# Performance work log

Hardware: AMD Instinct MI355X
Metric: run time of the kernel (lower is better)

The kernel has to match this reference:

```python
import jax, jax.numpy as jnp
import numpy as np

NEG = jnp.float32(-9e15)
SLOPE = 0.2  # LeakyReLU negative slope used in LocalAggregator


def setup_inputs() -> dict:
    key = jax.random.key(0)
    k1, k2, k3, k4, k5, k6, k7 = jax.random.split(key, 7)
    B, N, D, V = 32, 200, 100, 50000
    stdv = 1.0 / np.sqrt(D)
    inputs = jax.random.randint(k1, (B, N), 0, V)
    adj = jax.random.randint(k2, (B, N, N), 0, 5).astype(jnp.int32)
    mask_item = jnp.ones((B, N), dtype=jnp.int32)
    emb = jax.random.uniform(k3, (V, D), jnp.float32, -stdv, stdv)
    a0 = jax.random.uniform(k4, (D, 1), jnp.float32, -stdv, stdv)
    a1 = jax.random.uniform(k5, (D, 1), jnp.float32, -stdv, stdv)
    a2 = jax.random.uniform(k6, (D, 1), jnp.float32, -stdv, stdv)
    a3 = jax.random.uniform(k7, (D, 1), jnp.float32, -stdv, stdv)
    return {"inputs": inputs, "adj": adj, "mask_item": mask_item,
            "emb": emb, "a0": a0, "a1": a1, "a2": a2, "a3": a3}


def reference(inputs, adj, mask_item, emb, a0, a1, a2, a3):
    # h: [B, N, D] session item embeddings
    h = emb[inputs]
    # e_k[b,i,j] = leaky_relu(sum_d h[b,i,d]*h[b,j,d]*a_k[d])
    # (equivalent to the original (h_i * h_j) @ a_k without the BxNxNxD blowup)
    def edge_score(a):
        s = jnp.einsum('bid,bjd->bij', h * a[:, 0][None, None, :], h)
        return jax.nn.leaky_relu(s, SLOPE)
    e0, e1, e2, e3 = edge_score(a0), edge_score(a1), edge_score(a2), edge_score(a3)
    alpha = jnp.where(adj == 1, e0, NEG)
    alpha = jnp.where(adj == 2, e1, alpha)
    alpha = jnp.where(adj == 3, e2, alpha)
    alpha = jnp.where(adj == 4, e3, alpha)
    alpha = jax.nn.softmax(alpha, axis=-1)  # [B, N, N]
    # weighted aggregation over neighbors; dropout_local is inactive in eval
    return jnp.einsum('bij,bjd->bid', alpha, h)
```

## Files before the change

### kernel.cpp

```cpp
#include <hip/hip_runtime.h>
#include <math.h>

#define NEGV (-9e15f)
#define SLOPE 0.2f

__global__ __launch_bounds__(256, 1) void gat_tile_kernel(
    const int*   __restrict__ inputs,
    const int*   __restrict__ adj,
    const float* __restrict__ emb,
    const float* __restrict__ a0, const float* __restrict__ a1,
    const float* __restrict__ a2, const float* __restrict__ a3,
    float*       __restrict__ out)
{
    const int b   = blockIdx.x >> 3;
    const int i0  = (blockIdx.x & 7) * 25;
    const int tid = threadIdx.x;

    __shared__ int   sidx[200];
    __shared__ float G[25][4][100];
    __shared__ float ST[200][28];

    if (tid < 200) sidx[tid] = inputs[b * 200 + tid];
    __syncthreads();

    const float4* embv = (const float4*)emb;

    for (int t = tid; t < 25 * 25; t += 256) {
        const int i = t / 25, dc = t % 25;
        const float4 hv = embv[(size_t)sidx[i0 + i] * 25 + dc];
        const float4 av0 = ((const float4*)a0)[dc];
        const float4 av1 = ((const float4*)a1)[dc];
        const float4 av2 = ((const float4*)a2)[dc];
        const float4 av3 = ((const float4*)a3)[dc];
        float4 g;
        g.x=hv.x*av0.x; g.y=hv.y*av0.y; g.z=hv.z*av0.z; g.w=hv.w*av0.w;
        ((float4*)&G[i][0][0])[dc] = g;
        g.x=hv.x*av1.x; g.y=hv.y*av1.y; g.z=hv.z*av1.z; g.w=hv.w*av1.w;
        ((float4*)&G[i][1][0])[dc] = g;
        g.x=hv.x*av2.x; g.y=hv.y*av2.y; g.z=hv.z*av2.z; g.w=hv.w*av2.w;
        ((float4*)&G[i][2][0])[dc] = g;
        g.x=hv.x*av3.x; g.y=hv.y*av3.y; g.z=hv.z*av3.z; g.w=hv.w*av3.w;
        ((float4*)&G[i][3][0])[dc] = g;
    }

    float4 h[25];
    int    kv[25];
    if (tid < 200) {
        const size_t hb = (size_t)sidx[tid] * 25;
        #pragma unroll
        for (int c = 0; c < 25; ++c) h[c] = embv[hb + c];
        const int arow = (b * 200 + i0) * 200 + tid;
        #pragma unroll
        for (int i = 0; i < 25; ++i) kv[i] = adj[arow + i * 200];
    }
    __syncthreads();

    if (tid < 200) {
        for (int i = 0; i < 25; ++i) {
            const int k  = kv[i];
            const int kk = (k - 1) & 3;
            const float4* Gv = (const float4*)&G[i][kk][0];
            float ax = 0.f, ay = 0.f, az = 0.f, aw = 0.f;
            #pragma unroll
            for (int c = 0; c < 25; ++c) {
                const float4 gv = Gv[c];
                ax += gv.x * h[c].x; ay += gv.y * h[c].y;
                az += gv.z * h[c].z; aw += gv.w * h[c].w;
            }
            float s = (ax + ay) + (az + aw);
            s = (s >= 0.f) ? s : SLOPE * s;
            ST[tid][i] = (k >= 1 && k <= 4) ? s : NEGV;
        }
    }
    __syncthreads();

    {
        const int r = tid >> 3, l = tid & 7;
        if (r < 25) {
            float m = -INFINITY;
            #pragma unroll
            for (int t = 0; t < 25; ++t) m = fmaxf(m, ST[l + 8 * t][r]);
            #pragma unroll
            for (int off = 4; off >= 1; off >>= 1) m = fmaxf(m, __shfl_xor(m, off, 8));
            float e[25];
            float sum = 0.f;
            #pragma unroll
            for (int t = 0; t < 25; ++t) {
                e[t] = __expf(ST[l + 8 * t][r] - m);
                sum += e[t];
            }
            #pragma unroll
            for (int off = 4; off >= 1; off >>= 1) sum += __shfl_xor(sum, off, 8);
            const float inv = 1.0f / sum;
            #pragma unroll
            for (int t = 0; t < 25; ++t) ST[l + 8 * t][r] = e[t] * inv;
        }
    }
    __syncthreads();

    {
        const int ig = tid & 7;
        const int dc = tid >> 3;
        float4 acc[25];
        #pragma unroll
        for (int i = 0; i < 25; ++i) { acc[i].x = 0.f; acc[i].y = 0.f; acc[i].z = 0.f; acc[i].w = 0.f; }
        if (dc < 25) {
            for (int jj = 0; jj < 25; ++jj) {
                const int j = ig * 25 + jj;
                float4 w4[7];
                #pragma unroll
                for (int c = 0; c < 7; ++c) w4[c] = ((const float4*)&ST[j][0])[c];
                const float* w = (const float*)w4;
                const float4 hv = embv[(size_t)sidx[j] * 25 + dc];
                #pragma unroll
                for (int i = 0; i < 25; ++i) {
                    acc[i].x += w[i] * hv.x; acc[i].y += w[i] * hv.y;
                    acc[i].z += w[i] * hv.z; acc[i].w += w[i] * hv.w;
                }
            }
        }
        #pragma unroll
        for (int i = 0; i < 25; ++i) {
            #pragma unroll
            for (int off = 1; off <= 4; off <<= 1) {
                acc[i].x += __shfl_xor(acc[i].x, off, 64);
                acc[i].y += __shfl_xor(acc[i].y, off, 64);
                acc[i].z += __shfl_xor(acc[i].z, off, 64);
                acc[i].w += __shfl_xor(acc[i].w, off, 64);
            }
        }
        if (ig == 0 && dc < 25) {
            #pragma unroll
            for (int i = 0; i < 25; ++i)
                ((float4*)out)[(size_t)(b * 200 + i0 + i) * 25 + dc] = acc[i];
        }
    }
}

extern "C" void kernel_launch(void* const* d_in, const int* in_sizes, int n_in,
                              void* d_out, int out_size, void* d_ws, size_t ws_size,
                              hipStream_t stream) {
    const int*   inputs = (const int*)  d_in[0];
    const int*   adj    = (const int*)  d_in[1];
    const float* emb    = (const float*)d_in[3];
    const float* a0     = (const float*)d_in[4];
    const float* a1     = (const float*)d_in[5];
    const float* a2     = (const float*)d_in[6];
    const float* a3     = (const float*)d_in[7];
    float*       out    = (float*)d_out;

    gat_tile_kernel<<<dim3(256), dim3(256), 0, stream>>>(inputs, adj, emb, a0, a1, a2, a3, out);
}
```

Measured before the change: 111.3 us.

## Rewrite GAT kernel with fp16 MFMA scores and 16-row tiles

Replaces the scalar fp32 score computation with fp16 MFMA 16x16x32 matrix instructions over all four attention vectors, retiles to 16 query rows per block (416 blocks), caches the gathered embeddings as fp16 in shared memory, and stores softmax weights in fp16 for the aggregation step. The aim is to cut ALU time in the dot-product phase and raise grid occupancy. In exchange it computes four score matrices instead of selecting one per edge, and it loses precision in the scores, weights and embeddings.

Result: faster. 106.1 us (-4.7%).

```diff
diff --git a/kernel.cpp b/kernel.cpp
--- a/kernel.cpp
+++ b/kernel.cpp
@@ -1,10 +1,15 @@
 #include <hip/hip_runtime.h>
 #include <math.h>
 
-#define NEGV (-9e15f)
+#define NEGV  (-9e15f)
 #define SLOPE 0.2f
 
-__global__ __launch_bounds__(256, 1) void gat_tile_kernel(
+typedef __fp16 f16;
+typedef __fp16 f16x4 __attribute__((ext_vector_type(4)));
+typedef __fp16 f16x8 __attribute__((ext_vector_type(8)));
+typedef float  f32x4 __attribute__((ext_vector_type(4)));
+
+__global__ __launch_bounds__(256) void gat_mfma_kernel(
     const int*   __restrict__ inputs,
     const int*   __restrict__ adj,
     const float* __restrict__ emb,
@@ -12,127 +17,212 @@
     const float* __restrict__ a2, const float* __restrict__ a3,
     float*       __restrict__ out)
 {
-    const int b   = blockIdx.x >> 3;
-    const int i0  = (blockIdx.x & 7) * 25;
+    const int b   = blockIdx.x / 13;
+    const int i0  = (blockIdx.x % 13) * 16;
     const int tid = threadIdx.x;
 
+    __shared__ f16 HF[200][112];
+    __shared__ __align__(16) unsigned char ubuf[4 * 16 * 96 * 2];
+    __shared__ f16 GT[4][16][32];
     __shared__ int   sidx[200];
-    __shared__ float G[25][4][100];
-    __shared__ float ST[200][28];
-
-    if (tid < 200) sidx[tid] = inputs[b * 200 + tid];
-    __syncthreads();
-
-    const float4* embv = (const float4*)emb;
-
-    for (int t = tid; t < 25 * 25; t += 256) {
-        const int i = t / 25, dc = t % 25;
-        const float4 hv = embv[(size_t)sidx[i0 + i] * 25 + dc];
-        const float4 av0 = ((const float4*)a0)[dc];
-        const float4 av1 = ((const float4*)a1)[dc];
-        const float4 av2 = ((const float4*)a2)[dc];
-        const float4 av3 = ((const float4*)a3)[dc];
-        float4 g;
-        g.x=hv.x*av0.x; g.y=hv.y*av0.y; g.z=hv.z*av0.z; g.w=hv.w*av0.w;
-        ((float4*)&G[i][0][0])[dc] = g;
-        g.x=hv.x*av1.x; g.y=hv.y*av1.y; g.z=hv.z*av1.z; g.w=hv.w*av1.w;
-        ((float4*)&G[i][1][0])[dc] = g;
-        g.x=hv.x*av2.x; g.y=hv.y*av2.y; g.z=hv.z*av2.z; g.w=hv.w*av2.w;
-        ((float4*)&G[i][2][0])[dc] = g;
-        g.x=hv.x*av3.x; g.y=hv.y*av3.y; g.z=hv.z*av3.z; g.w=hv.w*av3.w;
-        ((float4*)&G[i][3][0])[dc] = g;
-    }
-
-    float4 h[25];
-    int    kv[25];
+    __shared__ float redmax[16][4];
+    __shared__ float redsum[16][4];
+
+    f16 (*GF)[16][96] = (f16(*)[16][96])ubuf;
+    f16 (*ST)[24]     = (f16(*)[24])ubuf;
+
+    for (int t = tid; t < 200; t += 256) sidx[t] = inputs[b * 200 + t];
+    __syncthreads();
+
     if (tid < 200) {
-        const size_t hb = (size_t)sidx[tid] * 25;
-        #pragma unroll
-        for (int c = 0; c < 25; ++c) h[c] = embv[hb + c];
-        const int arow = (b * 200 + i0) * 200 + tid;
-        #pragma unroll
-        for (int i = 0; i < 25; ++i) kv[i] = adj[arow + i * 200];
-    }
-    __syncthreads();
-
-    if (tid < 200) {
-        for (int i = 0; i < 25; ++i) {
-            const int k  = kv[i];
-            const int kk = (k - 1) & 3;
-            const float4* Gv = (const float4*)&G[i][kk][0];
-            float ax = 0.f, ay = 0.f, az = 0.f, aw = 0.f;
-            #pragma unroll
-            for (int c = 0; c < 25; ++c) {
-                const float4 gv = Gv[c];
-                ax += gv.x * h[c].x; ay += gv.y * h[c].y;
-                az += gv.z * h[c].z; aw += gv.w * h[c].w;
-            }
-            float s = (ax + ay) + (az + aw);
-            s = (s >= 0.f) ? s : SLOPE * s;
-            ST[tid][i] = (k >= 1 && k <= 4) ? s : NEGV;
-        }
-    }
-    __syncthreads();
-
-    {
-        const int r = tid >> 3, l = tid & 7;
-        if (r < 25) {
-            float m = -INFINITY;
-            #pragma unroll
-            for (int t = 0; t < 25; ++t) m = fmaxf(m, ST[l + 8 * t][r]);
-            #pragma unroll
-            for (int off = 4; off >= 1; off >>= 1) m = fmaxf(m, __shfl_xor(m, off, 8));
-            float e[25];
-            float sum = 0.f;
-            #pragma unroll
-            for (int t = 0; t < 25; ++t) {
-                e[t] = __expf(ST[l + 8 * t][r] - m);
-                sum += e[t];
-            }
-            #pragma unroll
-            for (int off = 4; off >= 1; off >>= 1) sum += __shfl_xor(sum, off, 8);
-            const float inv = 1.0f / sum;
-            #pragma unroll
-            for (int t = 0; t < 25; ++t) ST[l + 8 * t][r] = e[t] * inv;
-        }
-    }
-    __syncthreads();
-
-    {
-        const int ig = tid & 7;
-        const int dc = tid >> 3;
-        float4 acc[25];
-        #pragma unroll
-        for (int i = 0; i < 25; ++i) { acc[i].x = 0.f; acc[i].y = 0.f; acc[i].z = 0.f; acc[i].w = 0.f; }
-        if (dc < 25) {
-            for (int jj = 0; jj < 25; ++jj) {
-                const int j = ig * 25 + jj;
-                float4 w4[7];
-                #pragma unroll
-                for (int c = 0; c < 7; ++c) w4[c] = ((const float4*)&ST[j][0])[c];
-                const float* w = (const float*)w4;
-                const float4 hv = embv[(size_t)sidx[j] * 25 + dc];
-                #pragma unroll
-                for (int i = 0; i < 25; ++i) {
-                    acc[i].x += w[i] * hv.x; acc[i].y += w[i] * hv.y;
-                    acc[i].z += w[i] * hv.z; acc[i].w += w[i] * hv.w;
+        const float4* src = (const float4*)(emb + (size_t)sidx[tid] * 100);
+        f16x4* dst = (f16x4*)&HF[tid][0];
+        #pragma unroll
+        for (int c = 0; c < 25; ++c) {
+            const float4 v = src[c];
+            f16x4 o; o[0] = (f16)v.x; o[1] = (f16)v.y; o[2] = (f16)v.z; o[3] = (f16)v.w;
+            dst[c] = o;
+        }
+        const f16x4 z = {(f16)0.f, (f16)0.f, (f16)0.f, (f16)0.f};
+        dst[25] = z; dst[26] = z; dst[27] = z;
+    }
+
+    for (int t = tid; t < 4 * 16 * 24; t += 256) {
+        const int kk = t / (16 * 24);
+        const int rm = t % (16 * 24);
+        const int il = rm / 24;
+        const int c  = rm % 24;
+        const float* ak = (kk == 0) ? a0 : (kk == 1) ? a1 : (kk == 2) ? a2 : a3;
+        const int gi = i0 + il;
+        f16x4 o = {(f16)0.f, (f16)0.f, (f16)0.f, (f16)0.f};
+        if (gi < 200) {
+            const float4 hv = ((const float4*)(emb + (size_t)sidx[gi] * 100))[c];
+            const float4 av = ((const float4*)ak)[c];
+            o[0] = (f16)(hv.x * av.x); o[1] = (f16)(hv.y * av.y);
+            o[2] = (f16)(hv.z * av.z); o[3] = (f16)(hv.w * av.w);
+        }
+        ((f16x4*)&GF[kk][il][0])[c] = o;
+    }
+
+    for (int t = tid; t < 4 * 16 * 8; t += 256) {
+        const int kk = t / (16 * 8);
+        const int rm = t % (16 * 8);
+        const int il = rm / 8;
+        const int c  = rm % 8;
+        f16x4 o = {(f16)0.f, (f16)0.f, (f16)0.f, (f16)0.f};
+        const int gi = i0 + il;
+        if (c == 4 && gi < 200) {
+            const float* ak = (kk == 0) ? a0 : (kk == 1) ? a1 : (kk == 2) ? a2 : a3;
+            const float* hi = emb + (size_t)sidx[gi] * 100;
+            o[0] = (f16)(hi[96] * ak[96]); o[1] = (f16)(hi[97] * ak[97]);
+            o[2] = (f16)(hi[98] * ak[98]); o[3] = (f16)(hi[99] * ak[99]);
+        }
+        ((f16x4*)&GT[kk][il][0])[c] = o;
+    }
+    __syncthreads();
+
+    const int wave = tid >> 6;
+    const int lane = tid & 63;
+    const int lj   = lane & 15;
+    const int quad = lane >> 4;
+    const int rbase = quad * 4;
+
+    f32x4 acc[4][4];
+    #pragma unroll
+    for (int kk = 0; kk < 4; ++kk)
+        #pragma unroll
+        for (int jt = 0; jt < 4; ++jt)
+            acc[kk][jt] = (f32x4){0.f, 0.f, 0.f, 0.f};
+
+    #pragma unroll
+    for (int jtidx = 0; jtidx < 4; ++jtidx) {
+        const int j  = (wave + 4 * jtidx) * 16 + lj;
+        const int jr = (j < 200) ? j : 0;
+        const f16x8* Brow = (const f16x8*)&HF[jr][0];
+        const f16x8 b0 = Brow[quad];
+        const f16x8 b1 = Brow[4 + quad];
+        const f16x8 b2 = Brow[8 + quad];
+        const f16x8 b3 = Brow[10 + quad];
+        #pragma unroll
+        for (int kk = 0; kk < 4; ++kk) {
+            const f16x8* Arow = (const f16x8*)&GF[kk][lj][0];
+            f32x4 c = acc[kk][jtidx];
+            c = __builtin_amdgcn_mfma_f32_16x16x32_f16(Arow[quad],     b0, c, 0, 0, 0);
+            c = __builtin_amdgcn_mfma_f32_16x16x32_f16(Arow[4 + quad], b1, c, 0, 0, 0);
+            c = __builtin_amdgcn_mfma_f32_16x16x32_f16(Arow[8 + quad], b2, c, 0, 0, 0);
+            c = __builtin_amdgcn_mfma_f32_16x16x32_f16(((const f16x8*)&GT[kk][lj][0])[quad], b3, c, 0, 0, 0);
+            acc[kk][jtidx] = c;
+        }
+    }
+
+    float sel[4][4];
+    #pragma unroll
+    for (int jtidx = 0; jtidx < 4; ++jtidx) {
+        const int j = (wave + 4 * jtidx) * 16 + lj;
+        #pragma unroll
+        for (int reg = 0; reg < 4; ++reg) {
+            const int gi = i0 + rbase + reg;
+            float s = NEGV;
+            if (j < 200 && gi < 200) {
+                const int k = adj[(size_t)(b * 200 + gi) * 200 + j];
+                if (k >= 1 && k <= 4) {
+                    const float v = (k == 1) ? acc[0][jtidx][reg]
+                                  : (k == 2) ? acc[1][jtidx][reg]
+                                  : (k == 3) ? acc[2][jtidx][reg]
+                                  :            acc[3][jtidx][reg];
+                    s = (v >= 0.f) ? v : SLOPE * v;
                 }
             }
-        }
-        #pragma unroll
-        for (int i = 0; i < 25; ++i) {
-            #pragma unroll
-            for (int off = 1; off <= 4; off <<= 1) {
-                acc[i].x += __shfl_xor(acc[i].x, off, 64);
-                acc[i].y += __shfl_xor(acc[i].y, off, 64);
-                acc[i].z += __shfl_xor(acc[i].z, off, 64);
-                acc[i].w += __shfl_xor(acc[i].w, off, 64);
+            sel[jtidx][reg] = s;
+        }
+    }
+
+    #pragma unroll
+    for (int reg = 0; reg < 4; ++reg) {
+        float m = fmaxf(fmaxf(sel[0][reg], sel[1][reg]), fmaxf(sel[2][reg], sel[3][reg]));
+        #pragma unroll
+        for (int off = 1; off <= 8; off <<= 1) m = fmaxf(m, __shfl_xor(m, off, 16));
+        if (lj == 0) redmax[rbase + reg][wave] = m;
+    }
+    __syncthreads();
+    float m4[4], lsum[4];
+    #pragma unroll
+    for (int reg = 0; reg < 4; ++reg) {
+        const float* rr = redmax[rbase + reg];
+        m4[reg] = fmaxf(fmaxf(rr[0], rr[1]), fmaxf(rr[2], rr[3]));
+        lsum[reg] = 0.f;
+    }
+    float e[4][4];
+    #pragma unroll
+    for (int jtidx = 0; jtidx < 4; ++jtidx)
+        #pragma unroll
+        for (int reg = 0; reg < 4; ++reg) {
+            e[jtidx][reg] = __expf(sel[jtidx][reg] - m4[reg]);
+            lsum[reg] += e[jtidx][reg];
+        }
+    #pragma unroll
+    for (int reg = 0; reg < 4; ++reg) {
+        float s = lsum[reg];
+        #pragma unroll
+        for (int off = 1; off <= 8; off <<= 1) s += __shfl_xor(s, off, 16);
+        if (lj == 0) redsum[rbase + reg][wave] = s;
+    }
+    __syncthreads();
+    float inv[4];
+    #pragma unroll
+    for (int reg = 0; reg < 4; ++reg) {
+        const float* rr = redsum[rbase + reg];
+        inv[reg] = 1.0f / (rr[0] + rr[1] + rr[2] + rr[3]);
+    }
+    #pragma unroll
+    for (int jtidx = 0; jtidx < 4; ++jtidx) {
+        const int j = (wave + 4 * jtidx) * 16 + lj;
+        if (j < 200) {
+            #pragma unroll
+            for (int reg = 0; reg < 4; ++reg)
+                ST[j][rbase + reg] = (f16)(e[jtidx][reg] * inv[reg]);
+        }
+    }
+    __syncthreads();
+
+    const int ig = tid & 7;
+    const int dq = tid >> 3;
+    f32x4 o[16];
+    #pragma unroll
+    for (int i = 0; i < 16; ++i) o[i] = (f32x4){0.f, 0.f, 0.f, 0.f};
+    if (dq < 25) {
+        for (int jj = 0; jj < 25; ++jj) {
+            const int j = ig * 25 + jj;
+            const f16x8 w0 = *(const f16x8*)&ST[j][0];
+            const f16x8 w1 = *(const f16x8*)&ST[j][8];
+            const f16x4 hv = *(const f16x4*)&HF[j][dq * 4];
+            const float h0 = (float)hv[0], h1 = (float)hv[1],
+                        h2 = (float)hv[2], h3 = (float)hv[3];
+            #pragma unroll
+            for (int i = 0; i < 8; ++i) {
+                const float w = (float)w0[i];
+                o[i][0] += w * h0; o[i][1] += w * h1; o[i][2] += w * h2; o[i][3] += w * h3;
             }
-        }
-        if (ig == 0 && dc < 25) {
-            #pragma unroll
-            for (int i = 0; i < 25; ++i)
-                ((float4*)out)[(size_t)(b * 200 + i0 + i) * 25 + dc] = acc[i];
+            #pragma unroll
+            for (int i = 0; i < 8; ++i) {
+                const float w = (float)w1[i];
+                o[8 + i][0] += w * h0; o[8 + i][1] += w * h1; o[8 + i][2] += w * h2; o[8 + i][3] += w * h3;
+            }
+        }
+    }
+    #pragma unroll
+    for (int i = 0; i < 16; ++i)
+        #pragma unroll
+        for (int c = 0; c < 4; ++c)
+            #pragma unroll
+            for (int off = 1; off <= 4; off <<= 1)
+                o[i][c] += __shfl_xor(o[i][c], off, 8);
+    if (ig == 0 && dq < 25) {
+        #pragma unroll
+        for (int i = 0; i < 16; ++i) {
+            const int gi = i0 + i;
+            if (gi < 200)
+                ((f32x4*)out)[(size_t)(b * 200 + gi) * 25 + dq] = o[i];
         }
     }
 }
@@ -149,5 +239,5 @@
     const float* a3     = (const float*)d_in[7];
     float*       out    = (float*)d_out;
 
-    gat_tile_kernel<<<dim3(256), dim3(256), 0, stream>>>(inputs, adj, emb, a0, a1, a2, a3, out);
+    gat_mfma_kernel<<<dim3(32 * 13), dim3(256), 0, stream>>>(inputs, adj, emb, a0, a1, a2, a3, out);
 }
```
